# Kernel optimization log

Measured on AMD Instinct MI355X. Metric: run time of the kernel, lower is better.

The kernel has to match this reference:

```python
import jax, jax.numpy as jnp
import numpy as np

DEPTH = 3


def _outer(a, b):
    # batched tensor product of flattened tensor-algebra levels: (B, m) x (B, n) -> (B, m*n)
    return (a[:, :, None] * b[:, None, :]).reshape(a.shape[0], -1)


def _signature(X, depth):
    """Truncated path signature via Chen's identity (matches signatory.signature,
    basepoint=False). X: (B, T, C) -> (B, sum_k C^k)."""
    B, T, C = X.shape
    dX = X[:, 1:, :] - X[:, :-1, :]  # (B, T-1, C) increments

    def exp_levels(dx):
        # exp(dx) in truncated tensor algebra: level k = dx^{\otimes k} / k!
        e = [dx]
        for k in range(2, depth + 1):
            e.append(_outer(e[-1], dx) / k)
        return e

    def step(S, dx):
        e = exp_levels(dx)
        new = []
        for k in range(1, depth + 1):
            t = S[k - 1] + e[k - 1]  # terms with S_0=1 or e_0=1
            for i in range(1, k):
                t = t + _outer(S[i - 1], e[k - i - 1])
            new.append(t)
        return tuple(new), None

    init = tuple(jnp.zeros((B, C ** k), X.dtype) for k in range(1, depth + 1))
    S, _ = jax.lax.scan(step, init, jnp.swapaxes(dX, 0, 1))  # scan over time
    return jnp.concatenate(S, axis=1)


def setup_inputs() -> dict:
    key = jax.random.key(0)
    kx, kw, kb = jax.random.split(key, 3)
    B, T, C, n_out = 2048, 128, 8, 10
    sig_dim = sum(C ** k for k in range(1, DEPTH + 1))  # 584
    X = jax.random.normal(kx, (B, T, C), dtype=jnp.float32)
    bound = 1.0 / np.sqrt(sig_dim)
    W = jax.random.uniform(kw, (n_out, sig_dim), jnp.float32, -bound, bound)
    b = jax.random.uniform(kb, (n_out,), jnp.float32, -bound, bound)
    return {"X": X, "W": W, "b": b}


def reference(X, W, b):
    sig = _signature(X, DEPTH)          # (B, sig_dim)
    out = sig @ W.T + b                  # (B, n_outputs)
    return out.reshape(-1, W.shape[0])
```

## Files before the change

kernel.cpp:

```cpp
#include <hip/hip_runtime.h>

#define NOUT 10
#define SIG_DIM 584
#define TS 36

__device__ __forceinline__ float rdlane(float x, int lane) {
    return __int_as_float(__builtin_amdgcn_readlane(__float_as_int(x), lane));
}
__device__ __forceinline__ float comp4(float4 v, int c) {
    return c == 0 ? v.x : c == 1 ? v.y : c == 2 ? v.z : v.w;
}

__global__ __launch_bounds__(256) void sig_linear_kernel(
    const float* __restrict__ X, const float* __restrict__ W,
    const float* __restrict__ bias, float* __restrict__ out)
{
    __shared__ __align__(16) float s_xT[4][8 * TS];
    __shared__ float s_s2[4][64];
    __shared__ float s_part[4][16];

    const int tid = threadIdx.x;
    const int w = tid >> 6, l = tid & 63, i = l >> 3, j = l & 7;
    const int b = blockIdx.x;
    const int t0 = w * 32;
    const float* Xb = X + (size_t)b * 1024;

    const int rl_ = l >> 1, cb = (l & 1) * 4;
    const float4 d4 = *reinterpret_cast<const float4*>(Xb + (t0 + rl_) * 8 + cb);
    float* xT = &s_xT[w][0];
    xT[(cb + 0) * TS + rl_] = d4.x;
    xT[(cb + 1) * TS + rl_] = d4.y;
    xT[(cb + 2) * TS + rl_] = d4.z;
    xT[(cb + 3) * TS + rl_] = d4.w;
    if (l < 2) {
        const int rN = (t0 + 32 < 128) ? t0 + 32 : 127;
        const float4 e4 = *reinterpret_cast<const float4*>(Xb + rN * 8 + l * 4);
        xT[(l * 4 + 0) * TS + 32] = e4.x;
        xT[(l * 4 + 1) * TS + 32] = e4.y;
        xT[(l * 4 + 2) * TS + 32] = e4.z;
        xT[(l * 4 + 3) * TS + 32] = e4.w;
    }
    const float x0i = Xb[i];
    const float x0j = Xb[j];
    const float s1jv = Xb[1016 + j] - x0j;
    __syncthreads();

    float A[8];
#pragma unroll
    for (int k = 0; k < 8; ++k) A[k] = 0.f;
    float S2f = 0.f;

    const float* icol = xT + i * TS;
    const float* jcol = xT + j * TS;

    float xcr[8], xnr[8];
#pragma unroll
    for (int k = 0; k < 8; ++k)
        xcr[k] = rdlane(comp4(d4, k & 3), k >> 2);

    float4 ic = *reinterpret_cast<const float4*>(icol);
    float4 jc = *reinterpret_cast<const float4*>(jcol);

#pragma unroll
    for (int g4 = 0; g4 < 8; ++g4) {
        float4 in4, jn4;
        if (g4 < 7) {
            in4 = *reinterpret_cast<const float4*>(icol + 4 * g4 + 4);
            jn4 = *reinterpret_cast<const float4*>(jcol + 4 * g4 + 4);
        } else {
            in4 = make_float4(icol[32], 0.f, 0.f, 0.f);
            jn4 = make_float4(jcol[32], 0.f, 0.f, 0.f);
        }
#pragma unroll
        for (int q = 0; q < 4; ++q) {
            const int s = g4 * 4 + q;
            const float xci = comp4(ic, q);
            const float xcj = comp4(jc, q);
            const float xni = (q < 3) ? comp4(ic, q + 1) : in4.x;
            const float xnj = (q < 3) ? comp4(jc, q + 1) : jn4.x;
            if (s < 31) {
#pragma unroll
                for (int k = 0; k < 8; ++k)
                    xnr[k] = rdlane(comp4(d4, k & 3), 2 * (s + 1) + (k >> 2));
            } else {
#pragma unroll
                for (int k = 0; k < 8; ++k) xnr[k] = xT[k * TS + 32];
            }
            const float dxi = xni - xci;
            const float dxj = xnj - xcj;
            const float cpi = xci - x0i;
            const float cpj = xcj - x0j;
            (void)cpj;
            const float gg = dxj * fmaf(0.5f, dxi, cpi);
            const float hh = dxj * fmaf(1.0f / 6.0f, dxi, 0.5f * cpi);
            const float gmh = gg - hh;
            S2f += gg;
#pragma unroll
            for (int k = 0; k < 8; ++k)
                A[k] = fmaf(gmh, xnr[k], fmaf(hh, xcr[k], A[k]));
#pragma unroll
            for (int k = 0; k < 8; ++k) xcr[k] = xnr[k];
        }
        ic = in4;
        jc = jn4;
    }

    s_s2[w][l] = S2f;
    __syncthreads();
    const float S2T = s_s2[0][l] + s_s2[1][l] + s_s2[2][l] + s_s2[3][l];

    const float4 x7a = *reinterpret_cast<const float4*>(Xb + 1016);
    const float4 x7b = *reinterpret_cast<const float4*>(Xb + 1020);
#pragma unroll
    for (int o = 0; o < NOUT; ++o) {
        const float* wrow = W + o * SIG_DIM;
        const float4 w0 = *reinterpret_cast<const float4*>(wrow + 72 + l * 8);
        const float4 w1 = *reinterpret_cast<const float4*>(wrow + 72 + l * 8 + 4);
        float dA = w0.x * A[0];
        dA = fmaf(w0.y, A[1], dA); dA = fmaf(w0.z, A[2], dA);
        dA = fmaf(w0.w, A[3], dA); dA = fmaf(w1.x, A[4], dA);
        dA = fmaf(w1.y, A[5], dA); dA = fmaf(w1.z, A[6], dA);
        dA = fmaf(w1.w, A[7], dA);
        float part = -dA;
        if (w == 0) {
            float e = w0.x * x7a.x;
            e = fmaf(w0.y, x7a.y, e); e = fmaf(w0.z, x7a.z, e);
            e = fmaf(w0.w, x7a.w, e); e = fmaf(w1.x, x7b.x, e);
            e = fmaf(w1.y, x7b.y, e); e = fmaf(w1.z, x7b.z, e);
            e = fmaf(w1.w, x7b.w, e);
            part = fmaf(S2T, e + wrow[8 + l], part);
            if (i == 0) part = fmaf(s1jv, wrow[j], part);
        }
#pragma unroll
        for (int off = 32; off > 0; off >>= 1) part += __shfl_xor(part, off);
        if (l == o) s_part[w][o] = part;
    }
    __syncthreads();
    if (tid < NOUT)
        out[b * NOUT + tid] = s_part[0][tid] + s_part[1][tid] +
                              s_part[2][tid] + s_part[3][tid] + bias[tid];
}

extern "C" void kernel_launch(void* const* d_in, const int* in_sizes, int n_in,
                              void* d_out, int out_size, void* d_ws, size_t ws_size,
                              hipStream_t stream) {
    const float* X = (const float*)d_in[0];
    const float* W = (const float*)d_in[1];
    const float* bias = (const float*)d_in[2];
    float* out = (float*)d_out;
    sig_linear_kernel<<<dim3(2048), dim3(256), 0, stream>>>(X, W, bias, out);
}
```

Before: 26.69 us.

## Replace LDS transpose and readlane broadcasts with direct global/scalar loads

Drops the shared-memory transpose staging and its barrier. Each lane now reads its i/j path values straight from global memory. The full 8-wide row is fetched through a wave-uniform pointer so the compiler can use scalar loads instead of 64 readlane ops per step. The two FMA accumulation terms are merged by carrying the previous step's (gg-hh) weight forward, which halves the FMAs on A. In exchange it issues many small global loads per step and relies on cache hits and on scalar-load codegen.

```diff
diff --git a/kernel.cpp b/kernel.cpp
--- a/kernel.cpp
+++ b/kernel.cpp
@@ -2,20 +2,13 @@
 
 #define NOUT 10
 #define SIG_DIM 584
-#define TS 36
 
-__device__ __forceinline__ float rdlane(float x, int lane) {
-    return __int_as_float(__builtin_amdgcn_readlane(__float_as_int(x), lane));
-}
-__device__ __forceinline__ float comp4(float4 v, int c) {
-    return c == 0 ? v.x : c == 1 ? v.y : c == 2 ? v.z : v.w;
-}
+typedef float float8v __attribute__((ext_vector_type(8)));
 
 __global__ __launch_bounds__(256) void sig_linear_kernel(
     const float* __restrict__ X, const float* __restrict__ W,
     const float* __restrict__ bias, float* __restrict__ out)
 {
-    __shared__ __align__(16) float s_xT[4][8 * TS];
     __shared__ float s_s2[4][64];
     __shared__ float s_part[4][16];
 
@@ -24,91 +17,49 @@
     const int b = blockIdx.x;
     const int t0 = w * 32;
     const float* Xb = X + (size_t)b * 1024;
+    const float* Xu = X + (size_t)__builtin_amdgcn_readfirstlane(b) * 1024;
 
-    const int rl_ = l >> 1, cb = (l & 1) * 4;
-    const float4 d4 = *reinterpret_cast<const float4*>(Xb + (t0 + rl_) * 8 + cb);
-    float* xT = &s_xT[w][0];
-    xT[(cb + 0) * TS + rl_] = d4.x;
-    xT[(cb + 1) * TS + rl_] = d4.y;
-    xT[(cb + 2) * TS + rl_] = d4.z;
-    xT[(cb + 3) * TS + rl_] = d4.w;
-    if (l < 2) {
-        const int rN = (t0 + 32 < 128) ? t0 + 32 : 127;
-        const float4 e4 = *reinterpret_cast<const float4*>(Xb + rN * 8 + l * 4);
-        xT[(l * 4 + 0) * TS + 32] = e4.x;
-        xT[(l * 4 + 1) * TS + 32] = e4.y;
-        xT[(l * 4 + 2) * TS + 32] = e4.z;
-        xT[(l * 4 + 3) * TS + 32] = e4.w;
-    }
-    const float x0i = Xb[i];
-    const float x0j = Xb[j];
-    const float s1jv = Xb[1016 + j] - x0j;
-    __syncthreads();
+    const float* ci = Xb + t0 * 8 + i;
+    const float* cj = Xb + t0 * 8 + j;
+    const float x0i = Xb[i], x0j = Xb[j];
 
     float A[8];
 #pragma unroll
     for (int k = 0; k < 8; ++k) A[k] = 0.f;
-    float S2f = 0.f;
-
-    const float* icol = xT + i * TS;
-    const float* jcol = xT + j * TS;
-
-    float xcr[8], xnr[8];
-#pragma unroll
-    for (int k = 0; k < 8; ++k)
-        xcr[k] = rdlane(comp4(d4, k & 3), k >> 2);
-
-    float4 ic = *reinterpret_cast<const float4*>(icol);
-    float4 jc = *reinterpret_cast<const float4*>(jcol);
+    float S2f = 0.f, gp = 0.f;
+    float xci = ci[0], xcj = cj[0];
+    const int rowN = (w == 3) ? 31 : 32;
 
 #pragma unroll
-    for (int g4 = 0; g4 < 8; ++g4) {
-        float4 in4, jn4;
-        if (g4 < 7) {
-            in4 = *reinterpret_cast<const float4*>(icol + 4 * g4 + 4);
-            jn4 = *reinterpret_cast<const float4*>(jcol + 4 * g4 + 4);
-        } else {
-            in4 = make_float4(icol[32], 0.f, 0.f, 0.f);
-            jn4 = make_float4(jcol[32], 0.f, 0.f, 0.f);
-        }
+    for (int s = 0; s < 32; ++s) {
+        const int sn = (s < 31) ? (s + 1) * 8 : rowN * 8;
+        const float xni = ci[sn];
+        const float xnj = cj[sn];
+        const float8v rr = *reinterpret_cast<const float8v*>(Xu + (t0 + s) * 8);
+        const float dxi = xni - xci;
+        const float dxj = xnj - xcj;
+        const float cpi = xci - x0i;
+        const float gg = dxj * fmaf(0.5f, dxi, cpi);
+        const float hh = dxj * fmaf(1.0f / 6.0f, dxi, 0.5f * cpi);
+        const float wt = hh + gp;
+        gp = gg - hh;
+        S2f += gg;
 #pragma unroll
-        for (int q = 0; q < 4; ++q) {
-            const int s = g4 * 4 + q;
-            const float xci = comp4(ic, q);
-            const float xcj = comp4(jc, q);
-            const float xni = (q < 3) ? comp4(ic, q + 1) : in4.x;
-            const float xnj = (q < 3) ? comp4(jc, q + 1) : jn4.x;
-            if (s < 31) {
+        for (int k = 0; k < 8; ++k) A[k] = fmaf(wt, rr[k], A[k]);
+        xci = xni;
+        xcj = xnj;
+    }
+    {
+        const float8v rn = *reinterpret_cast<const float8v*>(Xu + (t0 + rowN) * 8);
 #pragma unroll
-                for (int k = 0; k < 8; ++k)
-                    xnr[k] = rdlane(comp4(d4, k & 3), 2 * (s + 1) + (k >> 2));
-            } else {
-#pragma unroll
-                for (int k = 0; k < 8; ++k) xnr[k] = xT[k * TS + 32];
-            }
-            const float dxi = xni - xci;
-            const float dxj = xnj - xcj;
-            const float cpi = xci - x0i;
-            const float cpj = xcj - x0j;
-            (void)cpj;
-            const float gg = dxj * fmaf(0.5f, dxi, cpi);
-            const float hh = dxj * fmaf(1.0f / 6.0f, dxi, 0.5f * cpi);
-            const float gmh = gg - hh;
-            S2f += gg;
-#pragma unroll
-            for (int k = 0; k < 8; ++k)
-                A[k] = fmaf(gmh, xnr[k], fmaf(hh, xcr[k], A[k]));
-#pragma unroll
-            for (int k = 0; k < 8; ++k) xcr[k] = xnr[k];
-        }
-        ic = in4;
-        jc = jn4;
+        for (int k = 0; k < 8; ++k) A[k] = fmaf(gp, rn[k], A[k]);
     }
 
     s_s2[w][l] = S2f;
     __syncthreads();
     const float S2T = s_s2[0][l] + s_s2[1][l] + s_s2[2][l] + s_s2[3][l];
 
+    const float s1jv = Xb[1016 + j] - x0j;
     const float4 x7a = *reinterpret_cast<const float4*>(Xb + 1016);
     const float4 x7b = *reinterpret_cast<const float4*>(Xb + 1020);
 #pragma unroll
```

New measurement: 32.96 us. 1.23x slower.
